# Performance work log

Hardware: AMD Instinct MI355X
Metric: run time of the kernel (lower is better)

Reference implementation:

```python
import jax, jax.numpy as jnp
import numpy as np

EMBED_DIM = 1024
NUM_HEADS = 16
HEAD_DIM = EMBED_DIM // NUM_HEADS


def setup_inputs() -> dict:
    key = jax.random.key(0)
    ks = jax.random.split(key, 5)
    s = 1.0 / np.sqrt(EMBED_DIM)
    x = jax.random.normal(ks[0], (2, 2048, EMBED_DIM), dtype=jnp.float32)
    wq = jax.random.normal(ks[1], (EMBED_DIM, EMBED_DIM), dtype=jnp.float32) * s
    wk = jax.random.normal(ks[2], (EMBED_DIM, EMBED_DIM), dtype=jnp.float32) * s
    wv = jax.random.normal(ks[3], (EMBED_DIM, EMBED_DIM), dtype=jnp.float32) * s
    wo = jax.random.normal(ks[4], (EMBED_DIM, EMBED_DIM), dtype=jnp.float32) * s
    z = jnp.zeros((EMBED_DIM,), dtype=jnp.float32)
    return {"x": x, "wq": wq, "bq": z, "wk": wk, "bk": z, "wv": wv, "bv": z, "wo": wo, "bo": z}


def reference(x, wq, bq, wk, bk, wv, bv, wo, bo):
    B, S, D = x.shape
    H, Hd = NUM_HEADS, HEAD_DIM
    # projections -> [B, H, S, Hd]
    def proj(w, b):
        return (x @ w + b).reshape(B, S, H, Hd).transpose(0, 2, 1, 3)
    q = proj(wq, bq)
    k = proj(wk, bk)
    v = proj(wv, bv)
    scores = jnp.einsum('bhsd,bhtd->bhst', q, k) / jnp.sqrt(jnp.float32(Hd))
    probs = jax.nn.softmax(scores, axis=-1)
    attn = jnp.einsum('bhst,bhtd->bhsd', probs, v)  # [B,H,S,Hd]
    attn = attn.transpose(0, 2, 1, 3).reshape(B, S, D)
    return attn @ wo + bo
```

## Files before the change

### kernel.cpp

```cpp
#include <hip/hip_runtime.h>
#include <cstdint>

typedef __bf16 bf16_t;
typedef __bf16 bf16x4 __attribute__((ext_vector_type(4)));
typedef __bf16 bf16x8 __attribute__((ext_vector_type(8)));
typedef float floatx4 __attribute__((ext_vector_type(4)));

#define EMBED 1024
#define NHEAD 16
#define HDIM  64
#define SEQ   2048
#define BATCH 2
#define MTOT  (BATCH*SEQ)
#define QSCALE 0.18033688011112042f

__device__ __forceinline__ void gload16(const bf16_t* g, bf16_t* l) {
    __builtin_amdgcn_global_load_lds(
        (const __attribute__((address_space(1))) void*)g,
        (__attribute__((address_space(3))) void*)l, 16, 0, 0);
}

__device__ __forceinline__ void drain_dma() {
    asm volatile("s_waitcnt vmcnt(0)" ::: "memory");
}

__global__ __launch_bounds__(256) void transpose4(
    const float* __restrict__ w0, const float* __restrict__ w1,
    const float* __restrict__ w2, const float* __restrict__ w3,
    const float* __restrict__ xin,
    bf16_t* __restrict__ out, bf16_t* __restrict__ xout)
{
    int z = blockIdx.z;
    int tx = threadIdx.x, ty = threadIdx.y;
    if (z >= 4) {
        const float* src = xin  + (size_t)(z - 4) * 1048576u;
        bf16_t*      dst = xout + (size_t)(z - 4) * 1048576u;
        int col = blockIdx.x * 32 + tx, rowb = blockIdx.y * 32;
#pragma unroll
        for (int j = 0; j < 4; j++) {
            int rr = rowb + ty + 8 * j;
            dst[(size_t)rr * 1024 + col] = (bf16_t)src[(size_t)rr * 1024 + col];
        }
        return;
    }
    __shared__ float t[32][33];
    const float* src = (z == 0) ? w0 : (z == 1) ? w1 : (z == 2) ? w2 : w3;
    bf16_t* dst = out + (size_t)z * 1048576u;
    int bx = blockIdx.x * 32, by = blockIdx.y * 32;
#pragma unroll
    for (int j = 0; j < 4; j++)
        t[ty + 8 * j][tx] = src[(size_t)(by + ty + 8 * j) * EMBED + bx + tx];
    __syncthreads();
#pragma unroll
    for (int j = 0; j < 4; j++)
        dst[(size_t)(bx + ty + 8 * j) * EMBED + by + tx] = (bf16_t)t[tx][ty + 8 * j];
}

template<int BM, int MODE>
__global__ __launch_bounds__(256) void gemm_t(
    const bf16_t* __restrict__ A,  const bf16_t* __restrict__ Bt,
    const float* __restrict__ bias0, const float* __restrict__ bias1,
    const float* __restrict__ bias2,
    void* __restrict__ outraw, bf16_t* __restrict__ vtout,
    int M, int N, int K)
{
    constexpr int MS = BM / 32;
    constexpr int BUFSZ = (BM + 128) * 64;
    __shared__ __align__(16) bf16_t smem[2 * BUFSZ];

    int tid  = threadIdx.x;
    int id   = blockIdx.x;
    int c8   = id & 7, rr_ = id >> 3;
    int nblk = N >> 7;
    int n0   = (rr_ % nblk) * 128;
    int m0   = ((rr_ / nblk) * 8 + c8) * BM;
    int wv   = tid >> 6, lane = tid & 63;
    int wr   = wv >> 1,  wc   = wv & 1;
    int quad = lane >> 4, l16 = lane & 15;
    int lr   = lane >> 3, lq = lane & 7;
    int sw   = (l16 & 7) * 8;
    int lcs  = ((lq ^ lr) * 8);

    floatx4 acc[MS][4];
    floatx4 z4 = {0.f, 0.f, 0.f, 0.f};
#pragma unroll
    for (int mi = 0; mi < MS; mi++)
#pragma unroll
        for (int ni = 0; ni < 4; ni++) acc[mi][ni] = z4;

    auto STAGE = [&](int k0, int buf) {
        bf16_t* as = smem + buf * BUFSZ;
        bf16_t* bs = as + BM * 64;
#pragma unroll
        for (int i = 0; i < BM / 32; i++) {
            int r = wv * (BM / 4) + i * 8;
            gload16(&A[(size_t)(m0 + r + lr) * K + k0 + lcs], as + r * 64);
        }
#pragma unroll
        for (int i = 0; i < 4; i++) {
            int r = wv * 32 + i * 8;
            gload16(&Bt[(size_t)(n0 + r + lr) * K + k0 + lcs], bs + r * 64);
        }
    };

    STAGE(0, 0);
    int T = K >> 6;
    for (int t = 0; t < T; t++) {
        int cur = t & 1;
        drain_dma();
        __syncthreads();
        if (t + 1 < T) STAGE((t + 1) << 6, cur ^ 1);
        bf16_t (*As)[64] = (bf16_t(*)[64])(smem + cur * BUFSZ);
        bf16_t (*Bs)[64] = (bf16_t(*)[64])(smem + cur * BUFSZ + BM * 64);
#pragma unroll
        for (int kk = 0; kk < 2; kk++) {
            bf16x8 af[MS], bfr[4];
            int co = kk * 32 + quad * 8;
#pragma unroll
            for (int i = 0; i < MS; i++)
                af[i]  = *(const bf16x8*)&As[wr * (BM / 2) + i * 16 + l16][co ^ sw];
#pragma unroll
            for (int i = 0; i < 4; i++)
                bfr[i] = *(const bf16x8*)&Bs[wc * 64 + i * 16 + l16][co ^ sw];
#pragma unroll
            for (int mi = 0; mi < MS; mi++)
#pragma unroll
                for (int ni = 0; ni < 4; ni++)
                    acc[mi][ni] = __builtin_amdgcn_mfma_f32_16x16x32_bf16(
                        af[mi], bfr[ni], acc[mi][ni], 0, 0, 0);
        }
    }

    if constexpr (MODE == 1) {
        if (n0 >= 2048) {
            bf16_t (*Ts)[72] = (bf16_t(*)[72])smem;
            int bb = m0 >> 11, s0 = m0 & 2047;
            int hd0 = n0 & 1023;
#pragma unroll
            for (int mh = 0; mh < 2; mh++) {
                __syncthreads();
                if (wr == mh) {
#pragma unroll
                    for (int mi = 0; mi < MS; mi++)
#pragma unroll
                        for (int ni = 0; ni < 4; ni++)
#pragma unroll
                            for (int r = 0; r < 4; r++) {
                                int ml = mi * 16 + quad * 4 + r;
                                int nl = wc * 64 + ni * 16 + l16;
                                float v = acc[mi][ni][r] + bias2[hd0 + nl];
                                int sp = ((ml >> 5) << 5) | (((ml >> 2) & 3) << 3)
                                       | (((ml >> 4) & 1) << 2) | (ml & 3);
                                Ts[nl][sp] = (bf16_t)v;
                            }
                }
                __syncthreads();
#pragma unroll
                for (int i = 0; i < 4; i++) {
                    int c = tid + i * 256;
                    int row = c >> 3, ch = (c & 7) * 8;
                    int hh = row >> 6, dd = row & 63;
                    size_t off = (((size_t)bb * NHEAD + (hd0 >> 6) + hh) * HDIM + dd) * SEQ
                               + (size_t)(s0 + mh * 64 + ch);
                    *(bf16x8*)&vtout[off] = *(const bf16x8*)&Ts[row][ch];
                }
            }
            return;
        }
    }

#pragma unroll
    for (int mi = 0; mi < MS; mi++) {
#pragma unroll
        for (int ni = 0; ni < 4; ni++) {
            int n = n0 + wc * 64 + ni * 16 + l16;
#pragma unroll
            for (int r = 0; r < 4; r++) {
                int m = m0 + wr * (BM / 2) + mi * 16 + quad * 4 + r;
                float v = acc[mi][ni][r];
                if (MODE == 0) {
                    ((float*)outraw)[(size_t)m * N + n] = v + bias0[n];
                } else {
                    int which = n >> 10, cc = n & 1023;
                    v += (which == 0) ? bias0[cc] : bias1[cc];
                    if (which == 0) v *= QSCALE;
                    int h = cc >> 6, d = cc & 63;
                    int b = m >> 11, s = m & 2047;
                    ((bf16_t*)outraw)[(size_t)which * 4194304u +
                        (((size_t)b * NHEAD + h) * SEQ + s) * HDIM + d] = (bf16_t)v;
                }
            }
        }
    }
}

__global__ __launch_bounds__(512) void attn_mfma(
    const bf16_t* __restrict__ Q, const bf16_t* __restrict__ K,
    const bf16_t* __restrict__ Vt, bf16_t* __restrict__ O)
{
    __shared__ __align__(16) bf16_t Ks[2][64][64];
    __shared__ __align__(16) bf16_t Vs[2][64][64];

    int tid  = threadIdx.x;
    int wv   = tid >> 6, lane = tid & 63;
    int quad = lane >> 4, l16 = lane & 15;
    int lr   = lane >> 3, lq = lane & 7;
    int sw   = (l16 & 7) * 8;
    int flat = blockIdx.x;
    int hb   = flat & 31;
    int qt   = flat >> 5;
    int h = hb & 15, b = hb >> 4;
    int bh = b * NHEAD + h;
    int qw = qt * 128 + wv * 16;

    const bf16_t* Qb = Q  + (size_t)bh * SEQ * HDIM;
    const bf16_t* Kb = K  + (size_t)bh * SEQ * HDIM;
    const bf16_t* Vb = Vt + (size_t)bh * SEQ * HDIM;

    int vwave = wv >> 2;
    int wr16  = (wv & 3) * 16;
    const bf16_t* sg = vwave
        ? Vb + (size_t)(wr16 + lr) * SEQ  + (lq ^ lr) * 8
        : Kb + (size_t)(wr16 + lr) * HDIM + (lq ^ lr) * 8;
    const size_t tstep = vwave ? 64u : 4096u;
    const size_t rstep = vwave ? 8u * SEQ : 8u * HDIM;

    auto STAGE = [&](int t, int buf) {
        const bf16_t* g = sg + (size_t)t * tstep;
        bf16_t* l = vwave ? &Vs[buf][wr16][0] : &Ks[buf][wr16][0];
        gload16(g, l);
        gload16(g + rstep, l + 8 * 64);
    };

    bf16x8 qf[2];
#pragma unroll
    for (int kk = 0; kk < 2; kk++)
        qf[kk] = *(const bf16x8*)
            &Qb[(size_t)(qw + l16) * HDIM + kk * 32 + quad * 8];

    floatx4 o_acc[4];
    floatx4 z4  = {0.f, 0.f, 0.f, 0.f};
    floatx4 m16 = {-16.f, -16.f, -16.f, -16.f};
#pragma unroll
    for (int nd = 0; nd < 4; nd++) o_acc[nd] = z4;
    float l_i = 0.f;

    STAGE(0, 0);

    for (int t = 0; t < 32; t++) {
        int cur = t & 1;
        drain_dma();
        __syncthreads();
        if (t < 31) STAGE(t + 1, cur ^ 1);

        floatx4 st[4];
#pragma unroll
        for (int ns = 0; ns < 4; ns++) st[ns] = m16;
        __builtin_amdgcn_s_setprio(1);
#pragma unroll
        for (int ns = 0; ns < 4; ns++) {
#pragma unroll
            for (int kk = 0; kk < 2; kk++) {
                bf16x8 kf = *(const bf16x8*)
                    &Ks[cur][ns * 16 + l16][(kk * 32 + quad * 8) ^ sw];
                st[ns] = __builtin_amdgcn_mfma_f32_16x16x32_bf16(
                    kf, qf[kk], st[ns], 0, 0, 0);
            }
        }
        __builtin_amdgcn_s_setprio(0);

        bf16x8 pf[2];
        float ls = 0.f;
#pragma unroll
        for (int kk = 0; kk < 2; kk++)
#pragma unroll
            for (int tt = 0; tt < 8; tt++) {
                float p = __builtin_amdgcn_exp2f(st[2 * kk + (tt >> 2)][tt & 3]);
                ls += p;
                pf[kk][tt] = (bf16_t)p;
            }
        l_i += ls;

        __builtin_amdgcn_s_setprio(1);
#pragma unroll
        for (int nd = 0; nd < 4; nd++) {
#pragma unroll
            for (int kk = 0; kk < 2; kk++) {
                bf16x8 vf = *(const bf16x8*)
                    &Vs[cur][nd * 16 + l16][(kk * 32 + quad * 8) ^ sw];
                o_acc[nd] = __builtin_amdgcn_mfma_f32_16x16x32_bf16(
                    vf, pf[kk], o_acc[nd], 0, 0, 0);
            }
        }
        __builtin_amdgcn_s_setprio(0);
    }

    float l = l_i;
    l += __shfl_xor(l, 16);
    l += __shfl_xor(l, 32);
    float inv = 1.f / l;
    int q = qw + l16;
    bf16_t* ob = O + ((size_t)b * SEQ + q) * EMBED + h * HDIM;
#pragma unroll
    for (int nd = 0; nd < 4; nd++)
#pragma unroll
        for (int r = 0; r < 4; r++)
            ob[nd * 16 + quad * 4 + r] = (bf16_t)(o_acc[nd][r] * inv);
}

extern "C" void kernel_launch(void* const* d_in, const int* in_sizes, int n_in,
                              void* d_out, int out_size, void* d_ws, size_t ws_size,
                              hipStream_t stream)
{
    const float* x  = (const float*)d_in[0];
    const float* wq = (const float*)d_in[1];
    const float* bq = (const float*)d_in[2];
    const float* wk = (const float*)d_in[3];
    const float* bk = (const float*)d_in[4];
    const float* wv = (const float*)d_in[5];
    const float* bv = (const float*)d_in[6];
    const float* wo = (const float*)d_in[7];
    const float* bo = (const float*)d_in[8];

    char*   ws    = (char*)d_ws;
    bf16_t* Wt    = (bf16_t*)ws;
    bf16_t* Xb    = (bf16_t*)(ws + 8ull  * 1024 * 1024);
    bf16_t* QKV   = (bf16_t*)(ws + 16ull * 1024 * 1024);
    bf16_t* Vt    = (bf16_t*)(ws + 40ull * 1024 * 1024);
    bf16_t* attnO = (bf16_t*)(ws + 48ull * 1024 * 1024);
    float*  outp  = (float*)d_out;

    transpose4<<<dim3(32, 32, 8), dim3(32, 8), 0, stream>>>(
        wq, wk, wv, wo, x, Wt, Xb);

    gemm_t<128, 1><<<dim3(768), 256, 0, stream>>>(
        Xb, Wt, bq, bk, bv, QKV, Vt, MTOT, 3072, EMBED);

    attn_mfma<<<dim3(512), 512, 0, stream>>>(
        QKV, QKV + 4194304u, Vt, attnO);

    gemm_t<64, 0><<<dim3(512), 256, 0, stream>>>(
        attnO, Wt + 3u * 1048576u, bo, bo, bo, outp, nullptr, MTOT, EMBED, EMBED);
}
```

Baseline: 179.7 us.

## Double attention KV tile to 128 keys per iteration with new staging swizzle

Processes 128 keys per main-loop iteration instead of 64, halving the number of barrier/drain steps. The K and V LDS tiles double in size, each wave issues four async global-to-LDS loads per stage, and the V tile uses a new XOR swizzle over 128 columns. It also adds a min-blocks hint of 4 to launch bounds, while doubling LDS use and score registers, which may affect occupancy.

```diff
diff --git a/kernel.cpp b/kernel.cpp
--- a/kernel.cpp
+++ b/kernel.cpp
@@ -194,18 +194,19 @@
     }
 }
 
-__global__ __launch_bounds__(512) void attn_mfma(
+__global__ __launch_bounds__(512, 4) void attn_mfma(
     const bf16_t* __restrict__ Q, const bf16_t* __restrict__ K,
     const bf16_t* __restrict__ Vt, bf16_t* __restrict__ O)
 {
-    __shared__ __align__(16) bf16_t Ks[2][64][64];
-    __shared__ __align__(16) bf16_t Vs[2][64][64];
+    __shared__ __align__(16) bf16_t Ks[2][128][64];
+    __shared__ __align__(16) bf16_t Vs[2][64][128];
 
     int tid  = threadIdx.x;
     int wv   = tid >> 6, lane = tid & 63;
     int quad = lane >> 4, l16 = lane & 15;
-    int lr   = lane >> 3, lq = lane & 7;
     int sw   = (l16 & 7) * 8;
+    int lr8  = lane >> 3, lq8  = lane & 7;
+    int lr16 = lane >> 4, lq16 = lane & 15;
     int flat = blockIdx.x;
     int hb   = flat & 31;
     int qt   = flat >> 5;
@@ -218,18 +219,29 @@
     const bf16_t* Vb = Vt + (size_t)bh * SEQ * HDIM;
 
     int vwave = wv >> 2;
-    int wr16  = (wv & 3) * 16;
-    const bf16_t* sg = vwave
-        ? Vb + (size_t)(wr16 + lr) * SEQ  + (lq ^ lr) * 8
-        : Kb + (size_t)(wr16 + lr) * HDIM + (lq ^ lr) * 8;
-    const size_t tstep = vwave ? 64u : 4096u;
-    const size_t rstep = vwave ? 8u * SEQ : 8u * HDIM;
+    const bf16_t* kgp = Kb + (size_t)(wv * 32 + lr8) * HDIM + (lq8 ^ lr8) * 8;
+    const bf16_t* vg0 = Vb + (size_t)((wv & 3) * 16 + lr16) * SEQ
+                           + (size_t)((lq16 ^ lr16) * 8);
+    const bf16_t* vg1 = Vb + (size_t)((wv & 3) * 16 + lr16) * SEQ
+                           + (size_t)((lq16 ^ (lr16 | 4)) * 8);
 
     auto STAGE = [&](int t, int buf) {
-        const bf16_t* g = sg + (size_t)t * tstep;
-        bf16_t* l = vwave ? &Vs[buf][wr16][0] : &Ks[buf][wr16][0];
-        gload16(g, l);
-        gload16(g + rstep, l + 8 * 64);
+        if (!vwave) {
+            const bf16_t* g = kgp + (size_t)t * (128u * HDIM);
+            bf16_t* l = &Ks[buf][wv * 32][0];
+            gload16(g,             l);
+            gload16(g +  8 * HDIM, l +  8 * 64);
+            gload16(g + 16 * HDIM, l + 16 * 64);
+            gload16(g + 24 * HDIM, l + 24 * 64);
+        } else {
+            const bf16_t* g0 = vg0 + (size_t)t * 128u;
+            const bf16_t* g1 = vg1 + (size_t)t * 128u;
+            bf16_t* l = &Vs[buf][(wv & 3) * 16][0];
+            gload16(g0,            l);
+            gload16(g1 +  4 * SEQ, l +  4 * 128);
+            gload16(g0 +  8 * SEQ, l +  8 * 128);
+            gload16(g1 + 12 * SEQ, l + 12 * 128);
+        }
     };
 
     bf16x8 qf[2];
@@ -247,18 +259,18 @@
 
     STAGE(0, 0);
 
-    for (int t = 0; t < 32; t++) {
+    for (int t = 0; t < 16; t++) {
         int cur = t & 1;
         drain_dma();
         __syncthreads();
-        if (t < 31) STAGE(t + 1, cur ^ 1);
-
-        floatx4 st[4];
-#pragma unroll
-        for (int ns = 0; ns < 4; ns++) st[ns] = m16;
+        if (t < 15) STAGE(t + 1, cur ^ 1);
+
+        floatx4 st[8];
+#pragma unroll
+        for (int ns = 0; ns < 8; ns++) st[ns] = m16;
         __builtin_amdgcn_s_setprio(1);
 #pragma unroll
-        for (int ns = 0; ns < 4; ns++) {
+        for (int ns = 0; ns < 8; ns++) {
 #pragma unroll
             for (int kk = 0; kk < 2; kk++) {
                 bf16x8 kf = *(const bf16x8*)
@@ -269,10 +281,10 @@
         }
         __builtin_amdgcn_s_setprio(0);
 
-        bf16x8 pf[2];
+        bf16x8 pf[4];
         float ls = 0.f;
 #pragma unroll
-        for (int kk = 0; kk < 2; kk++)
+        for (int kk = 0; kk < 4; kk++)
 #pragma unroll
             for (int tt = 0; tt < 8; tt++) {
                 float p = __builtin_amdgcn_exp2f(st[2 * kk + (tt >> 2)][tt & 3]);
@@ -285,9 +297,9 @@
 #pragma unroll
         for (int nd = 0; nd < 4; nd++) {
 #pragma unroll
-            for (int kk = 0; kk < 2; kk++) {
+            for (int kk = 0; kk < 4; kk++) {
                 bf16x8 vf = *(const bf16x8*)
-                    &Vs[cur][nd * 16 + l16][(kk * 32 + quad * 8) ^ sw];
+                    &Vs[cur][nd * 16 + l16][((kk * 4 + quad) ^ (l16 & 7)) << 3];
                 o_acc[nd] = __builtin_amdgcn_mfma_f32_16x16x32_bf16(
                     vf, pf[kk], o_acc[nd], 0, 0, 0);
             }
```

After: 174.6 us. 2.9% less time.
